# Performance work log

Measured on AMD Instinct MI355X. Metric: run time of the kernel, lower is better.

The kernel has to match this reference:

```python
import jax, jax.numpy as jnp
import numpy as np

IN_FEATURES = 4096
OUT_FEATURES = 4096
RANK = 32
ALPHA = 1.0
SCALE = ALPHA / RANK


def _kaiming_uniform(key, shape):
    # matches torch.nn.init.kaiming_uniform_(a=sqrt(5)) for a 2D weight:
    # gain = sqrt(2/(1+a^2)) = sqrt(1/3); bound = gain*sqrt(3/fan_in) = 1/sqrt(fan_in)
    fan_in = shape[1]  # torch fan_in of an (in_features, rank) tensor is shape[1]
    bound = 1.0 / np.sqrt(fan_in)
    return jax.random.uniform(key, shape, jnp.float32, -bound, bound)


def setup_inputs() -> dict:
    key = jax.random.key(0)
    kx, ka1, ka2, ka3 = jax.random.split(key, 4)
    x = jax.random.normal(kx, (4, 4096, IN_FEATURES), dtype=jnp.float32)
    A_fast = _kaiming_uniform(ka1, (IN_FEATURES, RANK))
    A_med = _kaiming_uniform(ka2, (IN_FEATURES, RANK))
    A_slow = _kaiming_uniform(ka3, (IN_FEATURES, RANK))
    # B matrices are zero-initialized in the module; use small random values so
    # the output is non-trivial for correctness checking.
    kb1, kb2, kb3 = jax.random.split(jax.random.fold_in(key, 7), 3)
    B_fast = 0.02 * jax.random.normal(kb1, (RANK, OUT_FEATURES), dtype=jnp.float32)
    B_med = 0.02 * jax.random.normal(kb2, (RANK, OUT_FEATURES), dtype=jnp.float32)
    B_slow = 0.02 * jax.random.normal(kb3, (RANK, OUT_FEATURES), dtype=jnp.float32)
    return {"x": x, "A_fast": A_fast, "B_fast": B_fast,
            "A_med": A_med, "B_med": B_med,
            "A_slow": A_slow, "B_slow": B_slow}


def reference(x, A_fast, B_fast, A_med, B_med, A_slow, B_slow):
    # Fused form: concat ranks -> two larger GEMMs, then scale.
    A = jnp.concatenate([A_fast, A_med, A_slow], axis=1)   # [in, 3r]
    B = jnp.concatenate([B_fast, B_med, B_slow], axis=0)   # [3r, out]
    h = jnp.einsum('bsi,ir->bsr', x, A)                    # [B, S, 3r]
    out = jnp.einsum('bsr,ro->bso', h, B) * SCALE          # [B, S, out]
    return out
```

## Files before the change

kernel.cpp:

```cpp
#include <hip/hip_runtime.h>
#include <hip/hip_bf16.h>

typedef __attribute__((ext_vector_type(4))) float f32x4;
typedef __attribute__((ext_vector_type(8))) short bf16x8;

__device__ __forceinline__ unsigned short f2bf(float f) {
  unsigned int u = __builtin_bit_cast(unsigned int, f);
  u += 0x7FFFu + ((u >> 16) & 1u);
  return (unsigned short)(u >> 16);
}

__device__ __forceinline__ void async_ld16(const void* g, void* l) {
  __builtin_amdgcn_global_load_lds(
      (__attribute__((address_space(1))) void*)g,
      (__attribute__((address_space(3))) void*)l, 16, 0, 0);
}

__global__ __launch_bounds__(256) void pack_AB(
    const float* __restrict__ Af, const float* __restrict__ Am,
    const float* __restrict__ As, const float* __restrict__ Bf,
    const float* __restrict__ Bm, const float* __restrict__ Bs,
    short* __restrict__ Apack, short* __restrict__ Bpack)
{
  unsigned idx = blockIdx.x * 256u + threadIdx.x;
  if (idx < 393216u) {
    unsigned j = idx & 7u, lane = (idx >> 3) & 63u, rest = idx >> 9;
    unsigned t = rest % 6u, chunk = rest / 6u;
    unsigned k = chunk * 32u + ((lane >> 4) << 3) + j;
    unsigned c = t * 16u + (lane & 15u);
    float v;
    if (c < 32u)      v = Af[k * 32u + c];
    else if (c < 64u) v = Am[k * 32u + (c - 32u)];
    else              v = As[k * 32u + (c - 64u)];
    Apack[idx] = (short)f2bf(v);
  } else {
    unsigned i2 = idx - 393216u;
    unsigned j = i2 & 7u, lane = (i2 >> 3) & 63u, rest = i2 >> 9;
    unsigned nt = rest & 255u, kc = rest >> 8;
    unsigned k = kc * 32u + ((lane >> 4) << 3) + j;
    unsigned n = nt * 16u + (lane & 15u);
    float v;
    if (k < 32u)      v = Bf[k * 4096u + n];
    else if (k < 64u) v = Bm[(k - 32u) * 4096u + n];
    else              v = Bs[(k - 64u) * 4096u + n];
    Bpack[i2] = (short)f2bf(v * 0.03125f);
  }
}

__global__ __launch_bounds__(256, 4) void lora_stage1(
    const float* __restrict__ x, const short* __restrict__ Apack,
    short* __restrict__ hg)
{
  const int rb  = blockIdx.x;
  const int tid = threadIdx.x;
  const int w = tid >> 6, l = tid & 63;
  const int lm = l & 15, lk = l >> 4;
  const size_t rowbase = (size_t)rb * 16;

  __shared__ __align__(16) float smem[8192];

  f32x4 acc[6];
#pragma unroll
  for (int t = 0; t < 6; ++t) acc[t] = (f32x4){0.f, 0.f, 0.f, 0.f};

  auto stage = [&](int s, int b) {
    float* base = smem + b * 4096;
    const float* gx = x + rowbase * 4096 + s * 256;
#pragma unroll
    for (int i = 0; i < 4; ++i) {
      int r = w * 4 + i;
      async_ld16(gx + (size_t)r * 4096 + ((l ^ (r & 7)) << 2), base + r * 256);
    }
  };

  auto consume = [&](int st) {
    const float* rowp = smem + (st & 1) * 4096 + lm * 256;
    const int sw = lm & 7;
#pragma unroll
    for (int p = 0; p < 2; ++p) {
      int ksub = w * 2 + p;
      int b0 = ksub * 8 + lk * 2;
      f32x4 xa = *(const f32x4*)(rowp + (((b0)     ^ sw) << 2));
      f32x4 xb = *(const f32x4*)(rowp + (((b0 + 1) ^ sw) << 2));
      bf16x8 xf;
      xf[0] = (short)f2bf(xa[0]); xf[1] = (short)f2bf(xa[1]);
      xf[2] = (short)f2bf(xa[2]); xf[3] = (short)f2bf(xa[3]);
      xf[4] = (short)f2bf(xb[0]); xf[5] = (short)f2bf(xb[1]);
      xf[6] = (short)f2bf(xb[2]); xf[7] = (short)f2bf(xb[3]);
      int kchunk = st * 8 + ksub;
#pragma unroll
      for (int t = 0; t < 6; ++t) {
        bf16x8 av = *(const bf16x8*)(Apack + ((size_t)kchunk * 6 + t) * 512 + l * 8);
        acc[t] = __builtin_amdgcn_mfma_f32_16x16x32_bf16(xf, av, acc[t], 0, 0, 0);
      }
    }
  };

  stage(0, 0);
#pragma unroll 1
  for (int st = 0; st < 15; ++st) {
    stage(st + 1, (st + 1) & 1);
    __builtin_amdgcn_sched_barrier(0);
    asm volatile("s_waitcnt vmcnt(4)" ::: "memory");
    __builtin_amdgcn_sched_barrier(0);
    __builtin_amdgcn_s_barrier();
    __builtin_amdgcn_sched_barrier(0);
    consume(st);
    __builtin_amdgcn_sched_barrier(0);
    __builtin_amdgcn_s_barrier();
    __builtin_amdgcn_sched_barrier(0);
  }
  asm volatile("s_waitcnt vmcnt(0)" ::: "memory");
  __builtin_amdgcn_sched_barrier(0);
  __builtin_amdgcn_s_barrier();
  __builtin_amdgcn_sched_barrier(0);
  consume(15);
  __syncthreads();

  {
    float* hpw = smem + w * 1600;
#pragma unroll
    for (int t = 0; t < 6; ++t)
#pragma unroll
      for (int q = 0; q < 4; ++q)
        hpw[(lk * 4 + q) * 100 + t * 16 + lm] = acc[t][q];
  }
  __syncthreads();

  if (tid < 192) {
    int r = tid / 12, c8 = tid % 12;
    const float* p = smem + r * 100 + c8 * 8;
    f32x4 s0 = *(const f32x4*)(p)        + *(const f32x4*)(p + 1600)
             + *(const f32x4*)(p + 3200) + *(const f32x4*)(p + 4800);
    f32x4 s1 = *(const f32x4*)(p + 4)    + *(const f32x4*)(p + 1604)
             + *(const f32x4*)(p + 3204) + *(const f32x4*)(p + 4804);
    bf16x8 o;
    o[0] = (short)f2bf(s0[0]); o[1] = (short)f2bf(s0[1]);
    o[2] = (short)f2bf(s0[2]); o[3] = (short)f2bf(s0[3]);
    o[4] = (short)f2bf(s1[0]); o[5] = (short)f2bf(s1[1]);
    o[6] = (short)f2bf(s1[2]); o[7] = (short)f2bf(s1[3]);
    *(bf16x8*)(hg + ((size_t)rb * 192 + (c8 >> 2) * 64 + (c8 & 3) * 16 + r) * 8) = o;
  }
}

__global__ __launch_bounds__(256, 4) void lora_stage2(
    const short* __restrict__ hg, const short* __restrict__ Bpack,
    float* __restrict__ out)
{
  const int bid = blockIdx.x;
  const int rs = bid >> 4;
  const int cb = bid & 15;
  const int tid = threadIdx.x;
  const int w = tid >> 6, l = tid & 63;
  const int lm = l & 15, lk = l >> 4;
  const int nt0 = cb * 16 + w * 4;

  bf16x8 bf[4][3];
#pragma unroll
  for (int n = 0; n < 4; ++n)
#pragma unroll
    for (int kc = 0; kc < 3; ++kc)
      bf[n][kc] = *(const bf16x8*)(Bpack + ((size_t)(kc * 256 + nt0 + n)) * 512 + l * 8);

#pragma unroll 2
  for (int it = 0; it < 8; ++it) {
    const int tile = rs * 8 + it;
    const short* hp = hg + (size_t)tile * 1536 + (size_t)l * 8;
    bf16x8 hf0 = *(const bf16x8*)(hp);
    bf16x8 hf1 = *(const bf16x8*)(hp + 512);
    bf16x8 hf2 = *(const bf16x8*)(hp + 1024);
    float* orow = out + ((size_t)tile * 16 + lm) * 4096;
#pragma unroll
    for (int n = 0; n < 4; ++n) {
      f32x4 a = {0.f, 0.f, 0.f, 0.f};
      a = __builtin_amdgcn_mfma_f32_16x16x32_bf16(bf[n][0], hf0, a, 0, 0, 0);
      a = __builtin_amdgcn_mfma_f32_16x16x32_bf16(bf[n][1], hf1, a, 0, 0, 0);
      a = __builtin_amdgcn_mfma_f32_16x16x32_bf16(bf[n][2], hf2, a, 0, 0, 0);
      *(f32x4*)(orow + (nt0 + n) * 16 + lk * 4) = a;
    }
  }
}

extern "C" void kernel_launch(void* const* d_in, const int* in_sizes, int n_in,
                              void* d_out, int out_size, void* d_ws, size_t ws_size,
                              hipStream_t stream) {
  const float* x  = (const float*)d_in[0];
  const float* Af = (const float*)d_in[1];
  const float* Bf = (const float*)d_in[2];
  const float* Am = (const float*)d_in[3];
  const float* Bm = (const float*)d_in[4];
  const float* As = (const float*)d_in[5];
  const float* Bs = (const float*)d_in[6];
  float* out = (float*)d_out;

  char* ws = (char*)d_ws;
  short* Apack = (short*)ws;
  short* Bpack = (short*)(ws + 786432);
  short* hg    = (short*)(ws + 2 * 786432);

  hipLaunchKernelGGL(pack_AB, dim3(3072), dim3(256), 0, stream,
                     Af, Am, As, Bf, Bm, Bs, Apack, Bpack);
  hipLaunchKernelGGL(lora_stage1, dim3(1024), dim3(256), 0, stream, x, Apack, hg);
  hipLaunchKernelGGL(lora_stage2, dim3(2048), dim3(256), 0, stream, hg, Bpack, out);
}
```

Before: 141.4 us.

## Split stage1 K dimension across two blocks and reduce partials in stage2

```diff
diff --git a/kernel.cpp b/kernel.cpp
--- a/kernel.cpp
+++ b/kernel.cpp
@@ -49,72 +49,85 @@
 
 __global__ __launch_bounds__(256, 4) void lora_stage1(
     const float* __restrict__ x, const short* __restrict__ Apack,
-    short* __restrict__ hg)
+    float* __restrict__ hg)
 {
-  const int rb  = blockIdx.x;
+  const int bid  = blockIdx.x;
+  const int tile = bid >> 1;
+  const int half = bid & 1;
   const int tid = threadIdx.x;
   const int w = tid >> 6, l = tid & 63;
   const int lm = l & 15, lk = l >> 4;
-  const size_t rowbase = (size_t)rb * 16;
-
-  __shared__ __align__(16) float smem[8192];
+  const size_t rowbase = (size_t)tile * 16;
+
+  __shared__ __align__(16) float smem[6400];
 
   f32x4 acc[6];
 #pragma unroll
   for (int t = 0; t < 6; ++t) acc[t] = (f32x4){0.f, 0.f, 0.f, 0.f};
 
   auto stage = [&](int s, int b) {
-    float* base = smem + b * 4096;
-    const float* gx = x + rowbase * 4096 + s * 256;
-#pragma unroll
-    for (int i = 0; i < 4; ++i) {
-      int r = w * 4 + i;
-      async_ld16(gx + (size_t)r * 4096 + ((l ^ (r & 7)) << 2), base + r * 256);
+    float* base = smem + b * 2048;
+    const float* gx = x + rowbase * 4096 + half * 2048 + s * 128;
+#pragma unroll
+    for (int i = 0; i < 2; ++i) {
+      int rp = w * 4 + i * 2;
+      int row = rp + (l >> 5);
+      int blk = (l & 31) ^ (row & 7);
+      async_ld16(gx + (size_t)row * 4096 + blk * 4, base + rp * 128);
     }
   };
 
-  auto consume = [&](int st) {
-    const float* rowp = smem + (st & 1) * 4096 + lm * 256;
+  auto consume = [&](int st, const bf16x8* av) {
+    const float* rowp = smem + (st & 1) * 2048 + lm * 128;
     const int sw = lm & 7;
-#pragma unroll
-    for (int p = 0; p < 2; ++p) {
-      int ksub = w * 2 + p;
-      int b0 = ksub * 8 + lk * 2;
-      f32x4 xa = *(const f32x4*)(rowp + (((b0)     ^ sw) << 2));
-      f32x4 xb = *(const f32x4*)(rowp + (((b0 + 1) ^ sw) << 2));
-      bf16x8 xf;
-      xf[0] = (short)f2bf(xa[0]); xf[1] = (short)f2bf(xa[1]);
-      xf[2] = (short)f2bf(xa[2]); xf[3] = (short)f2bf(xa[3]);
-      xf[4] = (short)f2bf(xb[0]); xf[5] = (short)f2bf(xb[1]);
-      xf[6] = (short)f2bf(xb[2]); xf[7] = (short)f2bf(xb[3]);
-      int kchunk = st * 8 + ksub;
-#pragma unroll
-      for (int t = 0; t < 6; ++t) {
-        bf16x8 av = *(const bf16x8*)(Apack + ((size_t)kchunk * 6 + t) * 512 + l * 8);
-        acc[t] = __builtin_amdgcn_mfma_f32_16x16x32_bf16(xf, av, acc[t], 0, 0, 0);
-      }
-    }
+    const int b0 = w * 8 + lk * 2;
+    f32x4 xa = *(const f32x4*)(rowp + ((b0 ^ sw) << 2));
+    f32x4 xb = *(const f32x4*)(rowp + (((b0 + 1) ^ sw) << 2));
+    bf16x8 xf;
+    xf[0] = (short)f2bf(xa[0]); xf[1] = (short)f2bf(xa[1]);
+    xf[2] = (short)f2bf(xa[2]); xf[3] = (short)f2bf(xa[3]);
+    xf[4] = (short)f2bf(xb[0]); xf[5] = (short)f2bf(xb[1]);
+    xf[6] = (short)f2bf(xb[2]); xf[7] = (short)f2bf(xb[3]);
+#pragma unroll
+    for (int t = 0; t < 6; ++t)
+      acc[t] = __builtin_amdgcn_mfma_f32_16x16x32_bf16(xf, av[t], acc[t], 0, 0, 0);
   };
 
   stage(0, 0);
 #pragma unroll 1
   for (int st = 0; st < 15; ++st) {
+    bf16x8 av[6];
+    {
+      const size_t kchunk = (size_t)(half * 64 + st * 4 + w);
+      const short* ap = Apack + kchunk * 3072 + (size_t)l * 8;
+#pragma unroll
+      for (int t = 0; t < 6; ++t) av[t] = *(const bf16x8*)(ap + t * 512);
+    }
+    __builtin_amdgcn_sched_barrier(0);
     stage(st + 1, (st + 1) & 1);
     __builtin_amdgcn_sched_barrier(0);
-    asm volatile("s_waitcnt vmcnt(4)" ::: "memory");
+    asm volatile("s_waitcnt vmcnt(2)" ::: "memory");
     __builtin_amdgcn_sched_barrier(0);
     __builtin_amdgcn_s_barrier();
     __builtin_amdgcn_sched_barrier(0);
-    consume(st);
+    consume(st, av);
     __builtin_amdgcn_sched_barrier(0);
     __builtin_amdgcn_s_barrier();
     __builtin_amdgcn_sched_barrier(0);
   }
-  asm volatile("s_waitcnt vmcnt(0)" ::: "memory");
-  __builtin_amdgcn_sched_barrier(0);
-  __builtin_amdgcn_s_barrier();
-  __builtin_amdgcn_sched_barrier(0);
-  consume(15);
+  {
+    bf16x8 av[6];
+    const size_t kchunk = (size_t)(half * 64 + 15 * 4 + w);
+    const short* ap = Apack + kchunk * 3072 + (size_t)l * 8;
+#pragma unroll
+    for (int t = 0; t < 6; ++t) av[t] = *(const bf16x8*)(ap + t * 512);
+    __builtin_amdgcn_sched_barrier(0);
+    asm volatile("s_waitcnt vmcnt(0)" ::: "memory");
+    __builtin_amdgcn_sched_barrier(0);
+    __builtin_amdgcn_s_barrier();
+    __builtin_amdgcn_sched_barrier(0);
+    consume(15, av);
+  }
   __syncthreads();
 
   {
@@ -134,17 +147,15 @@
              + *(const f32x4*)(p + 3200) + *(const f32x4*)(p + 4800);
     f32x4 s1 = *(const f32x4*)(p + 4)    + *(const f32x4*)(p + 1604)
              + *(const f32x4*)(p + 3204) + *(const f32x4*)(p + 4804);
-    bf16x8 o;
-    o[0] = (short)f2bf(s0[0]); o[1] = (short)f2bf(s0[1]);
-    o[2] = (short)f2bf(s0[2]); o[3] = (short)f2bf(s0[3]);
-    o[4] = (short)f2bf(s1[0]); o[5] = (short)f2bf(s1[1]);
-    o[6] = (short)f2bf(s1[2]); o[7] = (short)f2bf(s1[3]);
-    *(bf16x8*)(hg + ((size_t)rb * 192 + (c8 >> 2) * 64 + (c8 & 3) * 16 + r) * 8) = o;
-  }
-}
-
-__global__ __launch_bounds__(256, 4) void lora_stage2(
-    const short* __restrict__ hg, const short* __restrict__ Bpack,
+    float* dst = hg + ((size_t)half * 1024 + tile) * 1536
+               + (size_t)((c8 >> 2) * 64 + (c8 & 3) * 16 + r) * 8;
+    *(f32x4*)dst = s0;
+    *(f32x4*)(dst + 4) = s1;
+  }
+}
+
+__global__ __launch_bounds__(256, 6) void lora_stage2(
+    const float* __restrict__ hg, const short* __restrict__ Bpack,
     float* __restrict__ out)
 {
   const int bid = blockIdx.x;
@@ -165,17 +176,29 @@
 #pragma unroll 2
   for (int it = 0; it < 8; ++it) {
     const int tile = rs * 8 + it;
-    const short* hp = hg + (size_t)tile * 1536 + (size_t)l * 8;
-    bf16x8 hf0 = *(const bf16x8*)(hp);
-    bf16x8 hf1 = *(const bf16x8*)(hp + 512);
-    bf16x8 hf2 = *(const bf16x8*)(hp + 1024);
+    const float* hp0 = hg + (size_t)tile * 1536 + (size_t)l * 8;
+    const float* hp1 = hp0 + (size_t)1024 * 1536;
+    bf16x8 hf[3];
+#pragma unroll
+    for (int kc = 0; kc < 3; ++kc) {
+      f32x4 s0 = *(const f32x4*)(hp0 + kc * 512)
+               + *(const f32x4*)(hp1 + kc * 512);
+      f32x4 s1 = *(const f32x4*)(hp0 + kc * 512 + 4)
+               + *(const f32x4*)(hp1 + kc * 512 + 4);
+      bf16x8 o;
+      o[0] = (short)f2bf(s0[0]); o[1] = (short)f2bf(s0[1]);
+      o[2] = (short)f2bf(s0[2]); o[3] = (short)f2bf(s0[3]);
+      o[4] = (short)f2bf(s1[0]); o[5] = (short)f2bf(s1[1]);
+      o[6] = (short)f2bf(s1[2]); o[7] = (short)f2bf(s1[3]);
+      hf[kc] = o;
+    }
     float* orow = out + ((size_t)tile * 16 + lm) * 4096;
 #pragma unroll
     for (int n = 0; n < 4; ++n) {
       f32x4 a = {0.f, 0.f, 0.f, 0.f};
-      a = __builtin_amdgcn_mfma_f32_16x16x32_bf16(bf[n][0], hf0, a, 0, 0, 0);
-      a = __builtin_amdgcn_mfma_f32_16x16x32_bf16(bf[n][1], hf1, a, 0, 0, 0);
-      a = __builtin_amdgcn_mfma_f32_16x16x32_bf16(bf[n][2], hf2, a, 0, 0, 0);
+      a = __builtin_amdgcn_mfma_f32_16x16x32_bf16(bf[n][0], hf[0], a, 0, 0, 0);
+      a = __builtin_amdgcn_mfma_f32_16x16x32_bf16(bf[n][1], hf[1], a, 0, 0, 0);
+      a = __builtin_amdgcn_mfma_f32_16x16x32_bf16(bf[n][2], hf[2], a, 0, 0, 0);
       *(f32x4*)(orow + (nt0 + n) * 16 + lk * 4) = a;
     }
   }
@@ -196,10 +219,10 @@
   char* ws = (char*)d_ws;
   short* Apack = (short*)ws;
   short* Bpack = (short*)(ws + 786432);
-  short* hg    = (short*)(ws + 2 * 786432);
+  float* hg    = (float*)(ws + 2 * 786432);
 
   hipLaunchKernelGGL(pack_AB, dim3(3072), dim3(256), 0, stream,
                      Af, Am, As, Bf, Bm, Bs, Apack, Bpack);
-  hipLaunchKernelGGL(lora_stage1, dim3(1024), dim3(256), 0, stream, x, Apack, hg);
+  hipLaunchKernelGGL(lora_stage1, dim3(2048), dim3(256), 0, stream, x, Apack, hg);
   hipLaunchKernelGGL(lora_stage2, dim3(2048), dim3(256), 0, stream, hg, Bpack, out);
 }
```

New measurement: 261.5 us. +84.9%, slower.

## Replace LDS async loads with register-staged x prefetch in stage1 pipeline

Applied to the files above, without the earlier changes.

```diff
diff --git a/kernel.cpp b/kernel.cpp
--- a/kernel.cpp
+++ b/kernel.cpp
@@ -3,17 +3,13 @@
 
 typedef __attribute__((ext_vector_type(4))) float f32x4;
 typedef __attribute__((ext_vector_type(8))) short bf16x8;
+
+#define SBAR __builtin_amdgcn_sched_barrier(0)
 
 __device__ __forceinline__ unsigned short f2bf(float f) {
   unsigned int u = __builtin_bit_cast(unsigned int, f);
   u += 0x7FFFu + ((u >> 16) & 1u);
   return (unsigned short)(u >> 16);
-}
-
-__device__ __forceinline__ void async_ld16(const void* g, void* l) {
-  __builtin_amdgcn_global_load_lds(
-      (__attribute__((address_space(1))) void*)g,
-      (__attribute__((address_space(3))) void*)l, 16, 0, 0);
 }
 
 __global__ __launch_bounds__(256) void pack_AB(
@@ -51,70 +47,79 @@
     const float* __restrict__ x, const short* __restrict__ Apack,
     short* __restrict__ hg)
 {
-  const int rb  = blockIdx.x;
+  const int tile = blockIdx.x;
   const int tid = threadIdx.x;
   const int w = tid >> 6, l = tid & 63;
   const int lm = l & 15, lk = l >> 4;
-  const size_t rowbase = (size_t)rb * 16;
-
-  __shared__ __align__(16) float smem[8192];
+  const size_t rowbase = (size_t)tile * 16;
+
+  __shared__ __align__(16) float smem[6400];
 
   f32x4 acc[6];
 #pragma unroll
   for (int t = 0; t < 6; ++t) acc[t] = (f32x4){0.f, 0.f, 0.f, 0.f};
 
-  auto stage = [&](int s, int b) {
-    float* base = smem + b * 4096;
-    const float* gx = x + rowbase * 4096 + s * 256;
-#pragma unroll
-    for (int i = 0; i < 4; ++i) {
-      int r = w * 4 + i;
-      async_ld16(gx + (size_t)r * 4096 + ((l ^ (r & 7)) << 2), base + r * 256);
-    }
+  const int rp0 = w * 4 + (l >> 5);
+  const int rp1 = rp0 + 2;
+  const int cfl = (l & 31) * 4;
+  const float* g0 = x + (rowbase + rp0) * 4096 + cfl;
+  const float* g1 = x + (rowbase + rp1) * 4096 + cfl;
+  const int wp0 = rp0 * 128 + (((l & 31) ^ (rp0 & 7)) << 2);
+  const int wp1 = rp1 * 128 + (((l & 31) ^ (rp1 & 7)) << 2);
+
+#define XLOAD2(R0, R1, P0, P1)                                           \
+  asm volatile("global_load_dwordx4 %0, %2, off\n\t"                     \
+               "global_load_dwordx4 %1, %3, off"                         \
+               : "=&v"(R0), "=&v"(R1) : "v"(P0), "v"(P1) : "memory")
+
+  f32x4 xE0, xE1, xO0, xO1;
+
+  auto consume = [&](int st, const bf16x8* av) {
+    const float* rowp = smem + (st & 1) * 2048 + lm * 128;
+    const int sw = lm & 7;
+    const int b0 = w * 8 + lk * 2;
+    f32x4 xa = *(const f32x4*)(rowp + ((b0 ^ sw) << 2));
+    f32x4 xb = *(const f32x4*)(rowp + (((b0 + 1) ^ sw) << 2));
+    bf16x8 xf;
+    xf[0] = (short)f2bf(xa[0]); xf[1] = (short)f2bf(xa[1]);
+    xf[2] = (short)f2bf(xa[2]); xf[3] = (short)f2bf(xa[3]);
+    xf[4] = (short)f2bf(xb[0]); xf[5] = (short)f2bf(xb[1]);
+    xf[6] = (short)f2bf(xb[2]); xf[7] = (short)f2bf(xb[3]);
+#pragma unroll
+    for (int t = 0; t < 6; ++t)
+      acc[t] = __builtin_amdgcn_mfma_f32_16x16x32_bf16(xf, av[t], acc[t], 0, 0, 0);
   };
 
-  auto consume = [&](int st) {
-    const float* rowp = smem + (st & 1) * 4096 + lm * 256;
-    const int sw = lm & 7;
-#pragma unroll
-    for (int p = 0; p < 2; ++p) {
-      int ksub = w * 2 + p;
-      int b0 = ksub * 8 + lk * 2;
-      f32x4 xa = *(const f32x4*)(rowp + (((b0)     ^ sw) << 2));
-      f32x4 xb = *(const f32x4*)(rowp + (((b0 + 1) ^ sw) << 2));
-      bf16x8 xf;
-      xf[0] = (short)f2bf(xa[0]); xf[1] = (short)f2bf(xa[1]);
-      xf[2] = (short)f2bf(xa[2]); xf[3] = (short)f2bf(xa[3]);
-      xf[4] = (short)f2bf(xb[0]); xf[5] = (short)f2bf(xb[1]);
-      xf[6] = (short)f2bf(xb[2]); xf[7] = (short)f2bf(xb[3]);
-      int kchunk = st * 8 + ksub;
-#pragma unroll
-      for (int t = 0; t < 6; ++t) {
-        bf16x8 av = *(const bf16x8*)(Apack + ((size_t)kchunk * 6 + t) * 512 + l * 8);
-        acc[t] = __builtin_amdgcn_mfma_f32_16x16x32_bf16(xf, av, acc[t], 0, 0, 0);
-      }
-    }
-  };
-
-  stage(0, 0);
+#define STEP(ST, CUR0, CUR1, NXT0, NXT1, LAST) do {                      \
+    bf16x8 av[6];                                                        \
+    const short* ap = Apack + (size_t)((ST) * 4 + w) * 3072 + (size_t)l * 8; \
+    _Pragma("unroll")                                                    \
+    for (int t = 0; t < 6; ++t) av[t] = *(const bf16x8*)(ap + t * 512);  \
+    SBAR;                                                                \
+    if (!(LAST)) { XLOAD2(NXT0, NXT1, g0 + ((ST) + 1) * 128, g1 + ((ST) + 1) * 128); } \
+    SBAR;                                                                \
+    if (LAST) asm volatile("s_waitcnt vmcnt(0)" ::: "memory");           \
+    else      asm volatile("s_waitcnt vmcnt(2)" ::: "memory");           \
+    SBAR;                                                                \
+    { float* buf = smem + ((ST) & 1) * 2048;                             \
+      *(f32x4*)(buf + wp0) = CUR0; *(f32x4*)(buf + wp1) = CUR1; }        \
+    SBAR;                                                                \
+    asm volatile("s_waitcnt lgkmcnt(0)" ::: "memory");                   \
+    SBAR;                                                                \
+    __builtin_amdgcn_s_barrier();                                        \
+    SBAR;                                                                \
+    consume((ST), av);                                                   \
+    SBAR;                                                                \
+  } while (0)
+
+  XLOAD2(xE0, xE1, g0, g1);
 #pragma unroll 1
-  for (int st = 0; st < 15; ++st) {
-    stage(st + 1, (st + 1) & 1);
-    __builtin_amdgcn_sched_barrier(0);
-    asm volatile("s_waitcnt vmcnt(4)" ::: "memory");
-    __builtin_amdgcn_sched_barrier(0);
-    __builtin_amdgcn_s_barrier();
-    __builtin_amdgcn_sched_barrier(0);
-    consume(st);
-    __builtin_amdgcn_sched_barrier(0);
-    __builtin_amdgcn_s_barrier();
-    __builtin_amdgcn_sched_barrier(0);
-  }
-  asm volatile("s_waitcnt vmcnt(0)" ::: "memory");
-  __builtin_amdgcn_sched_barrier(0);
-  __builtin_amdgcn_s_barrier();
-  __builtin_amdgcn_sched_barrier(0);
-  consume(15);
+  for (int t2 = 0; t2 < 15; ++t2) {
+    STEP(2 * t2,     xE0, xE1, xO0, xO1, 0);
+    STEP(2 * t2 + 1, xO0, xO1, xE0, xE1, 0);
+  }
+  STEP(30, xE0, xE1, xO0, xO1, 0);
+  STEP(31, xO0, xO1, xE0, xE1, 1);
   __syncthreads();
 
   {
@@ -139,11 +144,11 @@
     o[2] = (short)f2bf(s0[2]); o[3] = (short)f2bf(s0[3]);
     o[4] = (short)f2bf(s1[0]); o[5] = (short)f2bf(s1[1]);
     o[6] = (short)f2bf(s1[2]); o[7] = (short)f2bf(s1[3]);
-    *(bf16x8*)(hg + ((size_t)rb * 192 + (c8 >> 2) * 64 + (c8 & 3) * 16 + r) * 8) = o;
-  }
-}
-
-__global__ __launch_bounds__(256, 4) void lora_stage2(
+    *(bf16x8*)(hg + ((size_t)tile * 192 + (c8 >> 2) * 64 + (c8 & 3) * 16 + r) * 8) = o;
+  }
+}
+
+__global__ __launch_bounds__(256, 8) void lora_stage2(
     const short* __restrict__ hg, const short* __restrict__ Bpack,
     float* __restrict__ out)
 {
```

New measurement: 228.8 us. +61.8%, slower.
